# Performance work log

Measured on AMD Instinct MI355X. Metric: run time of the kernel, lower is better.

## Reference

```python
import jax, jax.numpy as jnp
import numpy as np
import math

D_MODEL = 512
H = 8
D_K = D_MODEL // H


def setup_inputs() -> dict:
    key = jax.random.key(0)
    ks = jax.random.split(key, 12)
    B, T = 4, 1024
    q = jax.random.normal(ks[0], (B, T, D_MODEL), jnp.float32)
    k = jax.random.normal(ks[1], (B, T, D_MODEL), jnp.float32)
    v = jax.random.normal(ks[2], (B, T, D_MODEL), jnp.float32)
    mask = jnp.ones((B, T), jnp.int32)
    prev = jax.random.normal(ks[3], (B, H, T, T), jnp.float32)
    s = 1.0 / math.sqrt(D_MODEL)
    w_q = jax.random.normal(ks[4], (D_MODEL, D_MODEL), jnp.float32) * s
    w_k = jax.random.normal(ks[5], (D_MODEL, D_MODEL), jnp.float32) * s
    w_v = jax.random.normal(ks[6], (D_MODEL, D_MODEL), jnp.float32) * s
    w_o = jax.random.normal(ks[7], (D_MODEL, D_MODEL), jnp.float32) * s
    # Conv2d weights: torch layout OIHW; init std=0.01 per _init_conv_weights
    tw = jax.random.normal(ks[8], (H, H, 3, 3), jnp.float32) * 0.01
    tb = jnp.zeros((H,), jnp.float32)
    aw = jax.random.normal(ks[9], (H, 2 * H, 3, 3), jnp.float32) * 0.01
    ab = jnp.zeros((H,), jnp.float32)
    return {"q": q, "k": k, "v": v, "mask": mask, "previous_attention_scores": prev,
            "w_q": w_q, "w_k": w_k, "w_v": w_v, "w_o": w_o,
            "tw": tw, "tb": tb, "aw": aw, "ab": ab}


def _conv2d(x, w, b):
    # x: [B,C,T,T], w: [O,I,3,3] (torch OIHW), padding=1
    y = jax.lax.conv_general_dilated(
        x, w, window_strides=(1, 1), padding=((1, 1), (1, 1)),
        dimension_numbers=("NCHW", "OIHW", "NCHW"))
    return y + b[None, :, None, None]


def reference(q, k, v, mask, previous_attention_scores, w_q, w_k, w_v, w_o, tw, tb, aw, ab):
    B, T, _ = q.shape
    # torch Linear: y = x @ W^T  (W is [out,in])
    query = (q @ w_q.T).reshape(B, T, H, D_K).transpose(0, 2, 1, 3)  # [B,H,T,d_k]
    key = (k @ w_k.T).reshape(B, T, H, D_K).transpose(0, 2, 1, 3)
    value = (v @ w_v.T).reshape(B, T, H, D_K).transpose(0, 2, 1, 3)

    M = jnp.einsum("bhqd,bhkd->bhqk", query, key)  # [B,H,T,T]
    Mt = _conv2d(previous_attention_scores, tw, tb)
    Ma = _conv2d(jnp.concatenate((M, Mt), axis=1), aw, ab)

    A = Ma / math.sqrt(D_K)
    m = mask[:, None, None, :]  # [B,1,1,T]
    A = jnp.where(m == 0, -1e9, A)
    A = jax.nn.softmax(A, axis=-1)

    out = jnp.einsum("bhqk,bhkd->bhqd", A, value)
    out = out.transpose(0, 2, 1, 3).reshape(B, T, D_MODEL)
    return out @ w_o.T, A
```

## Files before the change

### kernel.cpp

```cpp
#include <hip/hip_runtime.h>
#include <hip/hip_bf16.h>

#define B_ 4
#define T_ 1024
#define DM 512
#define H_ 8
#define DK 64

typedef __attribute__((ext_vector_type(4))) float f32x4;
typedef __attribute__((ext_vector_type(8))) short bf16x8;

__device__ __forceinline__ unsigned short f2bf(float f) {
  __hip_bfloat16 h = __float2bfloat16(f);
  return *reinterpret_cast<unsigned short*>(&h);
}

template<int BLAY, int OMODE, int OUTBF>
__global__ __launch_bounds__(256)
void gemm64(const float* __restrict__ X, const float* __restrict__ W,
            void* __restrict__ outv, int M, int N, int K,
            long xbatch, long wbatch) {
  float* out = (float*)outv;
  unsigned short* outb = (unsigned short*)outv;
  __shared__ float Xs[16][68];
  __shared__ float Ws[16][68];
  const int t = threadIdx.x;
  const long bz = blockIdx.z;
  X += bz * xbatch;
  W += bz * wbatch;
  const int n0 = blockIdx.x * 64, m0 = blockIdx.y * 64;
  const int tx = t & 15, ty = t >> 4;
  float acc[4][4] = {};
  for (int k0 = 0; k0 < K; k0 += 16) {
    {
      int m = t >> 2, ks = (t & 3) << 2;
      float4 v = *(const float4*)&X[(long)(m0 + m) * K + k0 + ks];
      Xs[ks + 0][m] = v.x; Xs[ks + 1][m] = v.y;
      Xs[ks + 2][m] = v.z; Xs[ks + 3][m] = v.w;
    }
    if (BLAY == 0) {
      int n = t >> 2, ks = (t & 3) << 2;
      float4 v = *(const float4*)&W[(long)(n0 + n) * K + k0 + ks];
      Ws[ks + 0][n] = v.x; Ws[ks + 1][n] = v.y;
      Ws[ks + 2][n] = v.z; Ws[ks + 3][n] = v.w;
    } else {
      int r = t >> 4, cs = (t & 15) << 2;
      *(float4*)&Ws[r][cs] = *(const float4*)&W[(long)(k0 + r) * N + n0 + cs];
    }
    __syncthreads();
#pragma unroll
    for (int kk = 0; kk < 16; ++kk) {
      float a[4], b[4];
      *(float4*)a = *(const float4*)&Xs[kk][ty << 2];
      *(float4*)b = *(const float4*)&Ws[kk][tx << 2];
#pragma unroll
      for (int i = 0; i < 4; ++i)
#pragma unroll
        for (int j = 0; j < 4; ++j)
          acc[i][j] += a[i] * b[j];
    }
    __syncthreads();
  }
#pragma unroll
  for (int i = 0; i < 4; ++i) {
    int r = m0 + (ty << 2) + i;
    int c0 = n0 + (tx << 2);
    float4 v = make_float4(acc[i][0], acc[i][1], acc[i][2], acc[i][3]);
    if (OMODE == 0) {
      *(float4*)&out[(long)r * N + c0] = v;
    } else if (OMODE == 1) {
      int b = r >> 10, tt = r & 1023, h = c0 >> 6, d = c0 & 63;
      long off = ((long)(b * H_ + h) * T_ + tt) * DK + d;
      if (OUTBF) {
        uint2 pk;
        pk.x = (unsigned)f2bf(v.x) | ((unsigned)f2bf(v.y) << 16);
        pk.y = (unsigned)f2bf(v.z) | ((unsigned)f2bf(v.w) << 16);
        *(uint2*)&outb[off] = pk;
      } else {
        *(float4*)&out[off] = v;
      }
    } else {
      int b = (int)bz >> 3, h = (int)bz & 7;
      *(float4*)&out[(long)(b * T_ + r) * DM + h * DK + c0] = v;
    }
  }
}

__global__ __launch_bounds__(512, 4)
void fused_logits(const unsigned short* __restrict__ Qp,
                  const unsigned short* __restrict__ Kp,
                  const float* __restrict__ prev,
                  const float* __restrict__ tw, const float* __restrict__ tb,
                  const float* __restrict__ aw, const float* __restrict__ ab,
                  float* __restrict__ logits) {
  __shared__ __align__(16) unsigned short SM[34816];
  unsigned short* QKl = SM;
  unsigned short* C   = SM;
  unsigned short* P   = SM + 18496;

  const int t = threadIdx.x;
  const int b = blockIdx.z, q0 = blockIdx.y * 32, k0 = blockIdx.x * 32;
  const int wave = t >> 6, lane = t & 63;
  const int lrow = lane & 15, quad = lane >> 4;
  const int o = lrow;

  bf16x8 W2f[5], W1f[3];
#pragma unroll
  for (int ks = 0; ks < 5; ++ks) {
    int kk0 = ks * 32 + quad * 8;
    bf16x8 f = {0, 0, 0, 0, 0, 0, 0, 0};
    if (o < 8 && kk0 < 144) {
      int tap = kk0 >> 4, ib = kk0 & 15;
#pragma unroll
      for (int j = 0; j < 8; ++j)
        f[j] = (short)f2bf(aw[o * 144 + (ib + j) * 9 + tap]);
    }
    W2f[ks] = f;
  }
#pragma unroll
  for (int ks = 0; ks < 3; ++ks) {
    int kk0 = ks * 32 + quad * 8;
    bf16x8 f = {0, 0, 0, 0, 0, 0, 0, 0};
    if (o < 8 && kk0 < 72) {
      int tap = kk0 >> 3;
#pragma unroll
      for (int j = 0; j < 8; ++j)
        f[j] = (short)f2bf(tw[o * 72 + j * 9 + tap]);
    }
    W1f[ks] = f;
  }
  const float tb_r = (o < 8) ? tb[o] : 0.f;
  const float ab_r = (o < 8) ? ab[o] : 0.f;

  for (int c = t; c < 4352; c += 512) {
    int seg = c & 7;
    int rc = c >> 3;
    int ha = rc / 34;
    int row = rc - ha * 34;
    int h = ha >> 1, arr = ha & 1;
    int srow = (arr ? k0 : q0) - 1 + row;
    bf16x8 v = {0, 0, 0, 0, 0, 0, 0, 0};
    if (srow >= 0 && srow < T_) {
      const unsigned short* src =
          (arr ? Kp : Qp) + ((long)((b * H_ + h) * T_ + srow)) * DK + seg * 8;
      v = *(const bf16x8*)src;
    }
    *(bf16x8*)&QKl[rc * 64 + ((seg ^ (row & 7)) * 8)] = v;
  }
  __syncthreads();

  const int hp = wave & 3;
  const int hb = hp * 4;
  unsigned mbuf[5][4];
#pragma unroll
  for (int s = 0; s < 5; ++s) {
    int tile = (wave >> 2) + 2 * s;
    if (tile <= 8) {
      int ti = tile / 3, tj = tile - ti * 3;
      int rA = ti * 16 + lrow; rA = rA > 33 ? 33 : rA;
      int rB = tj * 16 + lrow; rB = rB > 33 ? 33 : rB;
      const unsigned short* pA0 = &QKl[((hb + 0) * 34 + rA) * 64];
      const unsigned short* pB0 = &QKl[((hb + 1) * 34 + rB) * 64];
      const unsigned short* pA1 = &QKl[((hb + 2) * 34 + rA) * 64];
      const unsigned short* pB1 = &QKl[((hb + 3) * 34 + rB) * 64];
      const int swA = rA & 7, swB = rB & 7;
      f32x4 acc0 = {0.f, 0.f, 0.f, 0.f};
      f32x4 acc1 = {0.f, 0.f, 0.f, 0.f};
#pragma unroll
      for (int c = 0; c < 2; ++c) {
        int sr = c * 4 + quad;
        bf16x8 a0 = *(const bf16x8*)&pA0[(sr ^ swA) * 8];
        bf16x8 b0 = *(const bf16x8*)&pB0[(sr ^ swB) * 8];
        acc0 = __builtin_amdgcn_mfma_f32_16x16x32_bf16(a0, b0, acc0, 0, 0, 0);
        bf16x8 a1 = *(const bf16x8*)&pA1[(sr ^ swA) * 8];
        bf16x8 b1 = *(const bf16x8*)&pB1[(sr ^ swB) * 8];
        acc1 = __builtin_amdgcn_mfma_f32_16x16x32_bf16(a1, b1, acc1, 0, 0, 0);
      }
#pragma unroll
      for (int r = 0; r < 4; ++r)
        mbuf[s][r] =
            (unsigned)f2bf(acc0[r]) | ((unsigned)f2bf(acc1[r]) << 16);
    }
  }
  __syncthreads();

#pragma unroll
  for (int s = 0; s < 5; ++s) {
    int tile = (wave >> 2) + 2 * s;
    if (tile <= 8) {
      int ti = tile / 3, tj = tile - ti * 3;
#pragma unroll
      for (int r = 0; r < 4; ++r) {
        int row = ti * 16 + quad * 4 + r, col = tj * 16 + lrow;
        if (row < 34 && col < 34) {
          int pix = row * 34 + col;
          int slot = pix ^ ((pix >> 2) & 3);
          *(unsigned*)&C[slot * 16 + (pix & 1) * 8 + hp * 2] = mbuf[s][r];
        }
      }
    }
  }

  for (int u = t; u < 648; u += 512) {
    int p2 = u * 2;
    int row = p2 / 36, col = p2 - row * 36;
    int gy = q0 - 2 + row, gx = k0 - 2 + col;
    bf16x8 v0 = {0, 0, 0, 0, 0, 0, 0, 0};
    bf16x8 v1 = {0, 0, 0, 0, 0, 0, 0, 0};
    if (gy >= 0 && gy < T_) {
      const float* src = prev + ((long)(b * H_) * T_ + gy) * T_ + gx;
      bool ia = (gx >= 0 && gx < T_), ib = (gx + 1 >= 0 && gx + 1 < T_);
      if (ia && ib) {
#pragma unroll
        for (int ch = 0; ch < 8; ++ch) {
          float2 w = *(const float2*)&src[(long)ch * T_ * T_];
          v0[ch] = (short)f2bf(w.x);
          v1[ch] = (short)f2bf(w.y);
        }
      } else {
        if (ia) {
#pragma unroll
          for (int ch = 0; ch < 8; ++ch)
            v0[ch] = (short)f2bf(src[(long)ch * T_ * T_]);
        }
        if (ib) {
#pragma unroll
          for (int ch = 0; ch < 8; ++ch)
            v1[ch] = (short)f2bf(src[(long)ch * T_ * T_ + 1]);
        }
      }
    }
    *(bf16x8*)&P[p2 * 8] = v0;
    *(bf16x8*)&P[(p2 + 1) * 8] = v1;
  }
  __syncthreads();

  for (int mt = wave; mt < 73; mt += 8) {
    int pin = mt * 16 + lrow;
    if (pin > 1155) pin = 1155;
    int yi = pin / 34, xi = pin - yi * 34;
    f32x4 acc = {0.f, 0.f, 0.f, 0.f};
#pragma unroll
    for (int ks = 0; ks < 3; ++ks) {
      int tap = ks * 4 + quad;
      if (tap > 8) tap = 8;
      int dy = tap / 3, dx = tap - dy * 3;
      bf16x8 av = *(const bf16x8*)&P[((yi + dy) * 36 + xi + dx) * 8];
      acc = __builtin_amdgcn_mfma_f32_16x16x32_bf16(av, W1f[ks], acc, 0, 0, 0);
    }
#pragma unroll
    for (int r = 0; r < 4; ++r) {
      int po = mt * 16 + quad * 4 + r;
      if (o < 8 && po < 1156) {
        int yo = po / 34, xo = po - yo * 34;
        int gy = q0 - 1 + yo, gx = k0 - 1 + xo;
        float val = (gy >= 0 && gy < T_ && gx >= 0 && gx < T_) ? acc[r] + tb_r
                                                               : 0.f;
        int slot = po ^ ((po >> 2) & 3);
        C[slot * 16 + ((po & 1) ^ 1) * 8 + o] = f2bf(val);
      }
    }
  }
  __syncthreads();

  for (int mt = wave; mt < 64; mt += 8) {
    int pin = mt * 16 + lrow;
    int yi = pin >> 5, xi = pin & 31;
    f32x4 acc = {0.f, 0.f, 0.f, 0.f};
#pragma unroll
    for (int ks = 0; ks < 5; ++ks) {
      int tap = ks * 2 + (quad >> 1);
      if (tap > 8) tap = 8;
      int dy = tap / 3, dx = tap - dy * 3;
      int p2 = (yi + dy) * 34 + (xi + dx);
      int slot = p2 ^ ((p2 >> 2) & 3);
      bf16x8 av =
          *(const bf16x8*)&C[slot * 16 + (((quad & 1) ^ (p2 & 1))) * 8];
      acc = __builtin_amdgcn_mfma_f32_16x16x32_bf16(av, W2f[ks], acc, 0, 0, 0);
    }
#pragma unroll
    for (int r = 0; r < 4; ++r) {
      int po = mt * 16 + quad * 4 + r;
      if (o < 8) {
        int yo = po >> 5, xo = po & 31;
        logits[((long)(b * H_ + o) * T_ + q0 + yo) * T_ + k0 + xo] =
            (acc[r] + ab_r) * 0.125f;
      }
    }
  }
}

__global__ __launch_bounds__(256)
void softmax_rows(float* __restrict__ A, const int* __restrict__ mask) {
  const int t = threadIdx.x;
  const int q = blockIdx.x, h = blockIdx.y, b = blockIdx.z;
  float* row = A + ((long)(b * H_ + h) * T_ + q) * T_;
  float4 v = *(float4*)&row[t * 4];
  int4 mv = *(const int4*)&mask[b * T_ + t * 4];
  v.x = (mv.x == 0) ? -1e9f : v.x;
  v.y = (mv.y == 0) ? -1e9f : v.y;
  v.z = (mv.z == 0) ? -1e9f : v.z;
  v.w = (mv.w == 0) ? -1e9f : v.w;

  __shared__ float r1[4], r2[4];
  const int wave = t >> 6, lane = t & 63;

  float mx4 = fmaxf(fmaxf(v.x, v.y), fmaxf(v.z, v.w));
  for (int of = 32; of > 0; of >>= 1) mx4 = fmaxf(mx4, __shfl_xor(mx4, of, 64));
  if (lane == 0) r1[wave] = mx4;
  __syncthreads();
  float mx = fmaxf(fmaxf(r1[0], r1[1]), fmaxf(r1[2], r1[3]));

  float e0 = __expf(v.x - mx), e1 = __expf(v.y - mx);
  float e2 = __expf(v.z - mx), e3 = __expf(v.w - mx);
  float s4 = (e0 + e1) + (e2 + e3);
  for (int of = 32; of > 0; of >>= 1) s4 += __shfl_xor(s4, of, 64);
  if (lane == 0) r2[wave] = s4;
  __syncthreads();
  float inv = 1.0f / (r2[0] + r2[1] + r2[2] + r2[3]);

  float4 ov;
  ov.x = e0 * inv; ov.y = e1 * inv; ov.z = e2 * inv; ov.w = e3 * inv;
  *(float4*)&row[t * 4] = ov;
}

extern "C" void kernel_launch(void* const* d_in, const int* in_sizes, int n_in,
                              void* d_out, int out_size, void* d_ws,
                              size_t ws_size, hipStream_t stream) {
  const float* q    = (const float*)d_in[0];
  const float* k    = (const float*)d_in[1];
  const float* v    = (const float*)d_in[2];
  const int*   mask = (const int*)  d_in[3];
  const float* prev = (const float*)d_in[4];
  const float* w_q  = (const float*)d_in[5];
  const float* w_k  = (const float*)d_in[6];
  const float* w_v  = (const float*)d_in[7];
  const float* w_o  = (const float*)d_in[8];
  const float* tw   = (const float*)d_in[9];
  const float* tb   = (const float*)d_in[10];
  const float* aw   = (const float*)d_in[11];
  const float* ab   = (const float*)d_in[12];

  float* out  = (float*)d_out;
  float* Aout = out + (long)B_ * T_ * DM;

  char* wsb = (char*)d_ws;
  unsigned short* Qp = (unsigned short*)wsb;
  unsigned short* Kp = (unsigned short*)(wsb + (4L << 20));
  float* Vp  = (float*)(wsb + (8L << 20));
  float* ctx = (float*)(wsb + (16L << 20));

  dim3 blk(256);

  gemm64<0, 1, 1><<<dim3(8, 64, 1), blk, 0, stream>>>(q, w_q, Qp, 4096, 512, 512, 0, 0);
  gemm64<0, 1, 1><<<dim3(8, 64, 1), blk, 0, stream>>>(k, w_k, Kp, 4096, 512, 512, 0, 0);
  gemm64<0, 1, 0><<<dim3(8, 64, 1), blk, 0, stream>>>(v, w_v, Vp, 4096, 512, 512, 0, 0);

  fused_logits<<<dim3(32, 32, 4), dim3(512), 0, stream>>>(Qp, Kp, prev, tw, tb,
                                                          aw, ab, Aout);

  softmax_rows<<<dim3(1024, 8, 4), blk, 0, stream>>>(Aout, mask);

  gemm64<1, 2, 0><<<dim3(1, 16, 32), blk, 0, stream>>>(Aout, Vp, ctx, 1024, 64, 1024,
                                                       (long)T_ * T_, (long)T_ * DK);

  gemm64<0, 0, 0><<<dim3(8, 64, 1), blk, 0, stream>>>(ctx, w_o, out, 4096, 512, 512, 0, 0);
}
```

Before: 716.0 us.

## Use split-bf16 MFMA GEMMs and fuse softmax with attention-value product

Replaces the scalar FP32 tiled GEMMs for the projections with MFMA kernels that split each fp32 operand into bf16 hi/lo parts and use three MFMAs per tile to keep near-fp32 accuracy. The separate softmax pass and the A@V GEMM are fused into one kernel. It computes row max and sum with an online pass, then normalizes, writes the probabilities back and feeds them to a split-bf16 MFMA product with V. The aim is to move the matmul work to matrix cores and avoid one extra full read and write of the attention matrix. In exchange the fused kernel reads each logits row twice, loads V with strided scalar reads, and has only 512 blocks.

```diff
diff --git a/kernel.cpp b/kernel.cpp
--- a/kernel.cpp
+++ b/kernel.cpp
@@ -15,75 +15,203 @@
   return *reinterpret_cast<unsigned short*>(&h);
 }
 
-template<int BLAY, int OMODE, int OUTBF>
+__device__ __forceinline__ void split2(float x, short& hi, short& lo) {
+  unsigned short h = f2bf(x);
+  float fh = __uint_as_float(((unsigned)h) << 16);
+  unsigned short l = f2bf(x - fh);
+  hi = (short)h; lo = (short)l;
+}
+
+template<int OMODE, int OUTBF>
 __global__ __launch_bounds__(256)
-void gemm64(const float* __restrict__ X, const float* __restrict__ W,
-            void* __restrict__ outv, int M, int N, int K,
-            long xbatch, long wbatch) {
+void proj_mfma(const float* __restrict__ X, const float* __restrict__ W,
+               void* __restrict__ outv, int M, int N, int K) {
   float* out = (float*)outv;
   unsigned short* outb = (unsigned short*)outv;
-  __shared__ float Xs[16][68];
-  __shared__ float Ws[16][68];
+  __shared__ __align__(16) unsigned short Ah[2048], Al[2048];
+  __shared__ __align__(16) unsigned short Bh[2048], Bl[2048];
   const int t = threadIdx.x;
-  const long bz = blockIdx.z;
-  X += bz * xbatch;
-  W += bz * wbatch;
   const int n0 = blockIdx.x * 64, m0 = blockIdx.y * 64;
-  const int tx = t & 15, ty = t >> 4;
-  float acc[4][4] = {};
-  for (int k0 = 0; k0 < K; k0 += 16) {
+  const int wave = t >> 6, lane = t & 63;
+  const int lrow = lane & 15, quad = lane >> 4;
+  const int wm = wave & 1, wn = wave >> 1;
+  const int srow = t >> 2, skc = t & 3;
+  const int sbase = srow * 32 + ((skc ^ ((srow >> 1) & 3)) * 8);
+  const int cswz = quad ^ ((lrow >> 1) & 3);
+  f32x4 acc[2][2] = {};
+
+  for (int k0 = 0; k0 < K; k0 += 32) {
     {
-      int m = t >> 2, ks = (t & 3) << 2;
-      float4 v = *(const float4*)&X[(long)(m0 + m) * K + k0 + ks];
-      Xs[ks + 0][m] = v.x; Xs[ks + 1][m] = v.y;
-      Xs[ks + 2][m] = v.z; Xs[ks + 3][m] = v.w;
-    }
-    if (BLAY == 0) {
-      int n = t >> 2, ks = (t & 3) << 2;
-      float4 v = *(const float4*)&W[(long)(n0 + n) * K + k0 + ks];
-      Ws[ks + 0][n] = v.x; Ws[ks + 1][n] = v.y;
-      Ws[ks + 2][n] = v.z; Ws[ks + 3][n] = v.w;
-    } else {
-      int r = t >> 4, cs = (t & 15) << 2;
-      *(float4*)&Ws[r][cs] = *(const float4*)&W[(long)(k0 + r) * N + n0 + cs];
+      const float* p = &X[(long)(m0 + srow) * K + k0 + skc * 8];
+      float4 v0 = *(const float4*)p, v1 = *(const float4*)(p + 4);
+      float xs[8] = {v0.x, v0.y, v0.z, v0.w, v1.x, v1.y, v1.z, v1.w};
+      bf16x8 hh, ll;
+#pragma unroll
+      for (int i = 0; i < 8; ++i) { short h, l; split2(xs[i], h, l); hh[i] = h; ll[i] = l; }
+      *(bf16x8*)&Ah[sbase] = hh; *(bf16x8*)&Al[sbase] = ll;
+    }
+    {
+      const float* p = &W[(long)(n0 + srow) * K + k0 + skc * 8];
+      float4 v0 = *(const float4*)p, v1 = *(const float4*)(p + 4);
+      float xs[8] = {v0.x, v0.y, v0.z, v0.w, v1.x, v1.y, v1.z, v1.w};
+      bf16x8 hh, ll;
+#pragma unroll
+      for (int i = 0; i < 8; ++i) { short h, l; split2(xs[i], h, l); hh[i] = h; ll[i] = l; }
+      *(bf16x8*)&Bh[sbase] = hh; *(bf16x8*)&Bl[sbase] = ll;
     }
     __syncthreads();
-#pragma unroll
-    for (int kk = 0; kk < 16; ++kk) {
-      float a[4], b[4];
-      *(float4*)a = *(const float4*)&Xs[kk][ty << 2];
-      *(float4*)b = *(const float4*)&Ws[kk][tx << 2];
-#pragma unroll
-      for (int i = 0; i < 4; ++i)
-#pragma unroll
-        for (int j = 0; j < 4; ++j)
-          acc[i][j] += a[i] * b[j];
-    }
+    bf16x8 ahv[2], alv[2], bhv[2], blv[2];
+#pragma unroll
+    for (int f = 0; f < 2; ++f) {
+      int ra = (wm * 32 + f * 16 + lrow) * 32 + cswz * 8;
+      ahv[f] = *(const bf16x8*)&Ah[ra];
+      alv[f] = *(const bf16x8*)&Al[ra];
+      int rb = (wn * 32 + f * 16 + lrow) * 32 + cswz * 8;
+      bhv[f] = *(const bf16x8*)&Bh[rb];
+      blv[f] = *(const bf16x8*)&Bl[rb];
+    }
+#pragma unroll
+    for (int fi = 0; fi < 2; ++fi)
+#pragma unroll
+      for (int fj = 0; fj < 2; ++fj) {
+        acc[fi][fj] = __builtin_amdgcn_mfma_f32_16x16x32_bf16(alv[fi], bhv[fj], acc[fi][fj], 0, 0, 0);
+        acc[fi][fj] = __builtin_amdgcn_mfma_f32_16x16x32_bf16(ahv[fi], blv[fj], acc[fi][fj], 0, 0, 0);
+        acc[fi][fj] = __builtin_amdgcn_mfma_f32_16x16x32_bf16(ahv[fi], bhv[fj], acc[fi][fj], 0, 0, 0);
+      }
     __syncthreads();
   }
-#pragma unroll
-  for (int i = 0; i < 4; ++i) {
-    int r = m0 + (ty << 2) + i;
-    int c0 = n0 + (tx << 2);
-    float4 v = make_float4(acc[i][0], acc[i][1], acc[i][2], acc[i][3]);
-    if (OMODE == 0) {
-      *(float4*)&out[(long)r * N + c0] = v;
-    } else if (OMODE == 1) {
-      int b = r >> 10, tt = r & 1023, h = c0 >> 6, d = c0 & 63;
-      long off = ((long)(b * H_ + h) * T_ + tt) * DK + d;
-      if (OUTBF) {
-        uint2 pk;
-        pk.x = (unsigned)f2bf(v.x) | ((unsigned)f2bf(v.y) << 16);
-        pk.y = (unsigned)f2bf(v.z) | ((unsigned)f2bf(v.w) << 16);
-        *(uint2*)&outb[off] = pk;
-      } else {
-        *(float4*)&out[off] = v;
-      }
-    } else {
-      int b = (int)bz >> 3, h = (int)bz & 7;
-      *(float4*)&out[(long)(b * T_ + r) * DM + h * DK + c0] = v;
-    }
-  }
+
+#pragma unroll
+  for (int fi = 0; fi < 2; ++fi)
+#pragma unroll
+    for (int fj = 0; fj < 2; ++fj)
+#pragma unroll
+      for (int r = 0; r < 4; ++r) {
+        int row = m0 + wm * 32 + fi * 16 + quad * 4 + r;
+        int col = n0 + wn * 32 + fj * 16 + lrow;
+        float v = acc[fi][fj][r];
+        if (OMODE == 0) {
+          out[(long)row * N + col] = v;
+        } else {
+          int b = row >> 10, tt = row & 1023, h = col >> 6, d = col & 63;
+          long off = ((long)(b * H_ + h) * T_ + tt) * DK + d;
+          if (OUTBF) outb[off] = f2bf(v);
+          else       out[off] = v;
+        }
+      }
+}
+
+__global__ __launch_bounds__(256)
+void softmax_av(float* __restrict__ A, const float* __restrict__ Vp,
+                float* __restrict__ ctx, const int* __restrict__ mask) {
+  __shared__ __align__(16) unsigned short Ah[2048], Al[2048];
+  __shared__ __align__(16) unsigned short Bh[2048], Bl[2048];
+  __shared__ float sm[64][4], ss[64][4];
+  const int t = threadIdx.x;
+  const int bh = blockIdx.y, b = bh >> 3, h = bh & 7;
+  const int m0 = blockIdx.x * 64;
+  A += (long)bh * T_ * T_;
+  const float* V = Vp + (long)bh * T_ * DK;
+  const int wave = t >> 6, lane = t & 63;
+  const int lrow = lane & 15, quad = lane >> 4;
+  const int wm = wave & 1, wn = wave >> 1;
+  const int srow = t >> 2, skc = t & 3;
+  float* arow_p = &A[(long)(m0 + srow) * T_];
+
+  float pm = -3.0e38f, ps = 0.f;
+  {
+    const int cb = skc * 256;
+    for (int c = 0; c < 256; c += 4) {
+      float4 v = *(const float4*)&arow_p[cb + c];
+      int4 mk = *(const int4*)&mask[b * T_ + cb + c];
+      float x0 = mk.x ? v.x : -1e9f;
+      float x1 = mk.y ? v.y : -1e9f;
+      float x2 = mk.z ? v.z : -1e9f;
+      float x3 = mk.w ? v.w : -1e9f;
+      float m4 = fmaxf(fmaxf(x0, x1), fmaxf(x2, x3));
+      if (m4 > pm) { ps *= __expf(pm - m4); pm = m4; }
+      ps += __expf(x0 - pm) + __expf(x1 - pm) + __expf(x2 - pm) + __expf(x3 - pm);
+    }
+  }
+  sm[srow][skc] = pm; ss[srow][skc] = ps;
+  __syncthreads();
+  const float rmx = fmaxf(fmaxf(sm[srow][0], sm[srow][1]),
+                          fmaxf(sm[srow][2], sm[srow][3]));
+  const float rsum = ss[srow][0] * __expf(sm[srow][0] - rmx)
+                   + ss[srow][1] * __expf(sm[srow][1] - rmx)
+                   + ss[srow][2] * __expf(sm[srow][2] - rmx)
+                   + ss[srow][3] * __expf(sm[srow][3] - rmx);
+  const float rinv = 1.0f / rsum;
+
+  const int sbase = srow * 32 + ((skc ^ ((srow >> 1) & 3)) * 8);
+  const int vn = t & 63, vkg = t >> 6;
+  const int bbase = vn * 32 + ((vkg ^ ((vn >> 1) & 3)) * 8);
+  const int cswz = quad ^ ((lrow >> 1) & 3);
+  f32x4 acc[2][2] = {};
+
+  for (int k0 = 0; k0 < T_; k0 += 32) {
+    __syncthreads();
+    {
+      float* p = &arow_p[k0 + skc * 8];
+      float4 v0 = *(const float4*)p, v1 = *(const float4*)(p + 4);
+      int4 mk0 = *(const int4*)&mask[b * T_ + k0 + skc * 8];
+      int4 mk1 = *(const int4*)&mask[b * T_ + k0 + skc * 8 + 4];
+      float e[8];
+      e[0] = __expf((mk0.x ? v0.x : -1e9f) - rmx) * rinv;
+      e[1] = __expf((mk0.y ? v0.y : -1e9f) - rmx) * rinv;
+      e[2] = __expf((mk0.z ? v0.z : -1e9f) - rmx) * rinv;
+      e[3] = __expf((mk0.w ? v0.w : -1e9f) - rmx) * rinv;
+      e[4] = __expf((mk1.x ? v1.x : -1e9f) - rmx) * rinv;
+      e[5] = __expf((mk1.y ? v1.y : -1e9f) - rmx) * rinv;
+      e[6] = __expf((mk1.z ? v1.z : -1e9f) - rmx) * rinv;
+      e[7] = __expf((mk1.w ? v1.w : -1e9f) - rmx) * rinv;
+      *(float4*)p = make_float4(e[0], e[1], e[2], e[3]);
+      *(float4*)(p + 4) = make_float4(e[4], e[5], e[6], e[7]);
+      bf16x8 hh, ll;
+#pragma unroll
+      for (int i = 0; i < 8; ++i) { short hi_, lo_; split2(e[i], hi_, lo_); hh[i] = hi_; ll[i] = lo_; }
+      *(bf16x8*)&Ah[sbase] = hh; *(bf16x8*)&Al[sbase] = ll;
+    }
+    {
+      bf16x8 hh, ll;
+#pragma unroll
+      for (int j = 0; j < 8; ++j) {
+        float x = V[(long)(k0 + vkg * 8 + j) * DK + vn];
+        short hi_, lo_; split2(x, hi_, lo_); hh[j] = hi_; ll[j] = lo_;
+      }
+      *(bf16x8*)&Bh[bbase] = hh; *(bf16x8*)&Bl[bbase] = ll;
+    }
+    __syncthreads();
+    bf16x8 ahv[2], alv[2], bhv[2], blv[2];
+#pragma unroll
+    for (int f = 0; f < 2; ++f) {
+      int ra = (wm * 32 + f * 16 + lrow) * 32 + cswz * 8;
+      ahv[f] = *(const bf16x8*)&Ah[ra];
+      alv[f] = *(const bf16x8*)&Al[ra];
+      int rb = (wn * 32 + f * 16 + lrow) * 32 + cswz * 8;
+      bhv[f] = *(const bf16x8*)&Bh[rb];
+      blv[f] = *(const bf16x8*)&Bl[rb];
+    }
+#pragma unroll
+    for (int fi = 0; fi < 2; ++fi)
+#pragma unroll
+      for (int fj = 0; fj < 2; ++fj) {
+        acc[fi][fj] = __builtin_amdgcn_mfma_f32_16x16x32_bf16(alv[fi], bhv[fj], acc[fi][fj], 0, 0, 0);
+        acc[fi][fj] = __builtin_amdgcn_mfma_f32_16x16x32_bf16(ahv[fi], blv[fj], acc[fi][fj], 0, 0, 0);
+        acc[fi][fj] = __builtin_amdgcn_mfma_f32_16x16x32_bf16(ahv[fi], bhv[fj], acc[fi][fj], 0, 0, 0);
+      }
+  }
+
+#pragma unroll
+  for (int fi = 0; fi < 2; ++fi)
+#pragma unroll
+    for (int fj = 0; fj < 2; ++fj)
+#pragma unroll
+      for (int r = 0; r < 4; ++r) {
+        int row = m0 + wm * 32 + fi * 16 + quad * 4 + r;
+        int col = wn * 32 + fj * 16 + lrow;
+        ctx[(long)(b * T_ + row) * DM + h * DK + col] = acc[fi][fj][r];
+      }
 }
 
 __global__ __launch_bounds__(512, 4)
@@ -288,40 +416,6 @@
       }
     }
   }
-}
-
-__global__ __launch_bounds__(256)
-void softmax_rows(float* __restrict__ A, const int* __restrict__ mask) {
-  const int t = threadIdx.x;
-  const int q = blockIdx.x, h = blockIdx.y, b = blockIdx.z;
-  float* row = A + ((long)(b * H_ + h) * T_ + q) * T_;
-  float4 v = *(float4*)&row[t * 4];
-  int4 mv = *(const int4*)&mask[b * T_ + t * 4];
-  v.x = (mv.x == 0) ? -1e9f : v.x;
-  v.y = (mv.y == 0) ? -1e9f : v.y;
-  v.z = (mv.z == 0) ? -1e9f : v.z;
-  v.w = (mv.w == 0) ? -1e9f : v.w;
-
-  __shared__ float r1[4], r2[4];
-  const int wave = t >> 6, lane = t & 63;
-
-  float mx4 = fmaxf(fmaxf(v.x, v.y), fmaxf(v.z, v.w));
-  for (int of = 32; of > 0; of >>= 1) mx4 = fmaxf(mx4, __shfl_xor(mx4, of, 64));
-  if (lane == 0) r1[wave] = mx4;
-  __syncthreads();
-  float mx = fmaxf(fmaxf(r1[0], r1[1]), fmaxf(r1[2], r1[3]));
-
-  float e0 = __expf(v.x - mx), e1 = __expf(v.y - mx);
-  float e2 = __expf(v.z - mx), e3 = __expf(v.w - mx);
-  float s4 = (e0 + e1) + (e2 + e3);
-  for (int of = 32; of > 0; of >>= 1) s4 += __shfl_xor(s4, of, 64);
-  if (lane == 0) r2[wave] = s4;
-  __syncthreads();
-  float inv = 1.0f / (r2[0] + r2[1] + r2[2] + r2[3]);
-
-  float4 ov;
-  ov.x = e0 * inv; ov.y = e1 * inv; ov.z = e2 * inv; ov.w = e3 * inv;
-  *(float4*)&row[t * 4] = ov;
 }
 
 extern "C" void kernel_launch(void* const* d_in, const int* in_sizes, int n_in,
@@ -352,17 +446,14 @@
 
   dim3 blk(256);
 
-  gemm64<0, 1, 1><<<dim3(8, 64, 1), blk, 0, stream>>>(q, w_q, Qp, 4096, 512, 512, 0, 0);
-  gemm64<0, 1, 1><<<dim3(8, 64, 1), blk, 0, stream>>>(k, w_k, Kp, 4096, 512, 512, 0, 0);
-  gemm64<0, 1, 0><<<dim3(8, 64, 1), blk, 0, stream>>>(v, w_v, Vp, 4096, 512, 512, 0, 0);
+  proj_mfma<1, 1><<<dim3(8, 64), blk, 0, stream>>>(q, w_q, Qp, 4096, 512, 512);
+  proj_mfma<1, 1><<<dim3(8, 64), blk, 0, stream>>>(k, w_k, Kp, 4096, 512, 512);
+  proj_mfma<1, 0><<<dim3(8, 64), blk, 0, stream>>>(v, w_v, Vp, 4096, 512, 512);
 
   fused_logits<<<dim3(32, 32, 4), dim3(512), 0, stream>>>(Qp, Kp, prev, tw, tb,
                                                           aw, ab, Aout);
 
-  softmax_rows<<<dim3(1024, 8, 4), blk, 0, stream>>>(Aout, mask);
-
-  gemm64<1, 2, 0><<<dim3(1, 16, 32), blk, 0, stream>>>(Aout, Vp, ctx, 1024, 64, 1024,
-                                                       (long)T_ * T_, (long)T_ * DK);
-
-  gemm64<0, 0, 0><<<dim3(8, 64, 1), blk, 0, stream>>>(ctx, w_o, out, 4096, 512, 512, 0, 0);
-}
+  softmax_av<<<dim3(16, 32), blk, 0, stream>>>(Aout, Vp, ctx, mask);
+
+  proj_mfma<0, 0><<<dim3(8, 64), blk, 0, stream>>>(ctx, w_o, out, 4096, 512, 512);
+}
```

Result: faster. 620.9 us (-13.3%).
